# Kernel optimization log

Hardware: AMD Instinct MI355X
Metric: run time of the kernel (lower is better)

Reference implementation:

```python
import jax, jax.numpy as jnp
import numpy as np

B, S, H = 2, 2048, 2048
NH, NKV, HD = 16, 4, 128
ROPE_BASE = 10000.0


def hbit_linear(x, w):
    # BitNet: 8-bit per-token absmax activation quant, ternary (2-bit) weight quant
    s = 127.0 / jnp.clip(jnp.max(jnp.abs(x), axis=-1, keepdims=True), 1e-5, None)
    xq = jnp.clip(jnp.round(x * s), -128, 127) / s
    ws = 1.0 / jnp.clip(jnp.mean(jnp.abs(w)), 1e-5, None)
    wq = jnp.clip(jnp.round(w * ws), -1, 1) / ws
    return xq @ wq.T


def rotate_half(x):
    h = x.shape[-1] // 2
    return jnp.concatenate([-x[..., h:], x[..., :h]], axis=-1)


def rope_cos_sin(position_ids, head_dim, dtype):
    inv_freq = 1.0 / (ROPE_BASE ** (jnp.arange(0, head_dim, 2, dtype=jnp.float32) / head_dim))
    freqs = position_ids.astype(jnp.float32)[..., None] * inv_freq[None, None, :]  # (b,s,hd/2)
    emb = jnp.concatenate([freqs, freqs], axis=-1)  # (b,s,hd)
    return jnp.cos(emb).astype(dtype)[:, :, None, :], jnp.sin(emb).astype(dtype)[:, :, None, :]


def setup_inputs() -> dict:
    key = jax.random.key(0)
    ks = jax.random.split(key, 5)
    xavier = lambda k, shp: jax.random.uniform(k, shp, jnp.float32, -1.0, 1.0) * np.sqrt(6.0 / (shp[0] + shp[1]))
    causal = jnp.where(jnp.tril(jnp.ones((S, S), bool)), 0.0, -1e9).astype(jnp.float32)[None, None]
    return {
        "hidden_states": jax.random.normal(ks[0], (B, S, H), jnp.float32),
        "attention_mask": causal,
        "Wq": xavier(ks[1], (H, H)),
        "Wk": xavier(ks[2], (NKV * HD, H)),
        "Wv": xavier(ks[3], (NKV * HD, H)),
        "Wo": xavier(ks[4], (H, H)),
        "position_ids": jnp.arange(S, dtype=jnp.int64 if jax.config.jax_enable_x64 else jnp.int32)[None, :],
    }


def reference(hidden_states, attention_mask, Wq, Wk, Wv, Wo, position_ids):
    b, s, _ = hidden_states.shape
    q = hbit_linear(hidden_states, Wq).reshape(b, s, NH, HD)
    k = hbit_linear(hidden_states, Wk).reshape(b, s, NKV, HD)
    v = hbit_linear(hidden_states, Wv).reshape(b, s, NKV, HD)
    cos, sin = rope_cos_sin(position_ids, HD, q.dtype)  # (1,s,1,hd)
    q = q * cos + rotate_half(q) * sin
    k = k * cos + rotate_half(k) * sin
    n_rep = NH // NKV
    k = jnp.repeat(k, n_rep, axis=2)  # (b,s,NH,hd)
    v = jnp.repeat(v, n_rep, axis=2)
    scale = 1.0 / np.sqrt(HD)
    scores = jnp.einsum("bqhd,bkhd->bhqk", q, k) * scale + attention_mask
    probs = jax.nn.softmax(scores, axis=-1)  # dropout inactive (eval)
    out = jnp.einsum("bhqk,bkhd->bqhd", probs, v).reshape(b, s, NH * HD)
    return hbit_linear(out, Wo)
```

## Files before the change

kernel.cpp:

```cpp
#include <hip/hip_runtime.h>
#include <hip/hip_bf16.h>

#define B_ 2
#define S_ 2048
#define H_ 2048
#define NH_ 16
#define NKV_ 4
#define HD_ 128
#define M_ (B_*S_)
#define KVD_ (NKV_*HD_)

typedef signed char s8;
typedef __attribute__((ext_vector_type(8))) short short8;
typedef __attribute__((ext_vector_type(4))) float f32x4;
typedef __attribute__((ext_vector_type(4))) int int4v;

__device__ __forceinline__ float loadf(const void* p, long i, int isb){
  if (isb) return __bfloat162float(((const __hip_bfloat16*)p)[i]);
  return ((const float*)p)[i];
}

__device__ __forceinline__ unsigned short f2bf(float f){
  union { float f; unsigned u; } v; v.f = f;
  unsigned r = v.u + 0x7FFF + ((v.u >> 16) & 1);
  return (unsigned short)(r >> 16);
}

__device__ __forceinline__ float bf2f(unsigned short b){
  union { unsigned u; float f; } v; v.u = ((unsigned)b) << 16; return v.f;
}

__device__ __forceinline__ void gl2lds16(const void* g, void* l){
  __builtin_amdgcn_global_load_lds(
      (const __attribute__((address_space(1))) void*)g,
      (__attribute__((address_space(3))) void*)l, 16, 0, 0);
}

__global__ void k_detect(const unsigned int* x, int* flag){
  __shared__ int sh[256];
  int t = threadIdx.x, c = 0;
  for (int i = t; i < 2048; i += 256){
    unsigned e = (x[i] >> 7) & 0xFF;
    if (e >= 90 && e <= 150) c++;
  }
  sh[t] = c; __syncthreads();
  for (int k = 128; k > 0; k >>= 1){ if (t < k) sh[t] += sh[t+k]; __syncthreads(); }
  if (t == 0) flag[0] = (sh[0] > 1228) ? 1 : 0;
}

__global__ void k_prep(const void* Wq, const void* Wk, const void* Wv, const void* Wo,
                       const int* flag, float* wsum, float* ct, float* st){
  int bid = blockIdx.x, t = threadIdx.x;
  if (t < 64){
    float inv = exp2f(-(float)t * 0.20762050593045952f);
    float a = (float)bid * inv;
    float sn, cs; sincosf(a, &sn, &cs);
    ct[bid*64 + t] = cs; st[bid*64 + t] = sn;
  }
  __shared__ float sh[256];
  int isb = *flag;
  const void* w; long n; int wi; long b0; int nb;
  if (bid < 768)       { w = Wq; wi = 0; n = (long)H_*H_;   b0 = bid;      nb = 768; }
  else if (bid < 1024) { w = Wk; wi = 1; n = (long)KVD_*H_; b0 = bid-768;  nb = 256; }
  else if (bid < 1280) { w = Wv; wi = 2; n = (long)KVD_*H_; b0 = bid-1024; nb = 256; }
  else                 { w = Wo; wi = 3; n = (long)H_*H_;   b0 = bid-1280; nb = 768; }
  float s = 0.f;
  for (long i = b0*256 + t; i < n; i += (long)nb*256) s += fabsf(loadf(w, i, isb));
  sh[t] = s; __syncthreads();
  for (int k = 128; k > 0; k >>= 1){ if (t < k) sh[t] += sh[t+k]; __syncthreads(); }
  if (t == 0) atomicAdd(&wsum[wi], sh[0]);
}

__global__ void k_wquant_all(const void* Wq, const void* Wk, const void* Wv, const void* Wo,
                             const int* flag, const float* wsum,
                             s8* oq, s8* ok, s8* ov, s8* oo){
  int isb = *flag;
  int bid = blockIdx.x, t = threadIdx.x;
  const float cntq = (float)((long)H_*H_), cntkv = (float)((long)KVD_*H_);
  const void* w; s8* out; long n; int wi; long b0; int nb; float cnt;
  if (bid < 1024)      { w = Wq; out = oq; wi = 0; n = (long)H_*H_;   b0 = bid;       nb = 1024; cnt = cntq; }
  else if (bid < 1280) { w = Wk; out = ok; wi = 1; n = (long)KVD_*H_; b0 = bid-1024;  nb = 256;  cnt = cntkv; }
  else if (bid < 1536) { w = Wv; out = ov; wi = 2; n = (long)KVD_*H_; b0 = bid-1280;  nb = 256;  cnt = cntkv; }
  else                 { w = Wo; out = oo; wi = 3; n = (long)H_*H_;   b0 = bid-1536;  nb = 1024; cnt = cntq; }
  float mean = fmaxf(wsum[wi] / cnt, 1e-5f);
  float sc = 1.0f / mean;
  for (long i = b0*256 + t; i < n; i += (long)nb*256){
    float v = rintf(loadf(w, i, isb) * sc);
    v = fminf(fmaxf(v, -1.f), 1.f);
    out[i] = (s8)v;
  }
}

__global__ void k_aquant_in(const void* x, const int* flag, float* srow, s8* xq){
  __shared__ float sh[256];
  int isb = *flag; int r = blockIdx.x, t = threadIdx.x;
  long base = (long)r * H_;
  float v[8];
  if (isb){
    uint4 wv = ((const uint4*)((const unsigned short*)x + base))[t];
    unsigned u[4] = {wv.x, wv.y, wv.z, wv.w};
    #pragma unroll
    for (int i = 0; i < 4; i++){
      v[2*i]   = bf2f((unsigned short)(u[i] & 0xFFFF));
      v[2*i+1] = bf2f((unsigned short)(u[i] >> 16));
    }
  } else {
    const float4* p = (const float4*)((const float*)x + base);
    float4 a = p[t*2], b2 = p[t*2+1];
    v[0]=a.x; v[1]=a.y; v[2]=a.z; v[3]=a.w; v[4]=b2.x; v[5]=b2.y; v[6]=b2.z; v[7]=b2.w;
  }
  float mx = 0.f;
  #pragma unroll
  for (int i = 0; i < 8; i++) mx = fmaxf(mx, fabsf(v[i]));
  sh[t] = mx; __syncthreads();
  for (int k = 128; k > 0; k >>= 1){ if (t < k) sh[t] = fmaxf(sh[t], sh[t+k]); __syncthreads(); }
  float s = 127.0f / fmaxf(sh[0], 1e-5f);
  if (t == 0) srow[r] = s;
  unsigned long long pk = 0;
  #pragma unroll
  for (int i = 0; i < 8; i++){
    float q = fminf(fmaxf(rintf(v[i] * s), -128.f), 127.f);
    pk |= ((unsigned long long)(unsigned char)(s8)q) << (8*i);
  }
  *(unsigned long long*)(xq + base + t*8) = pk;
}

__global__ void k_aquant_bf16(const unsigned short* __restrict__ x, float* __restrict__ srow, s8* __restrict__ xq){
  __shared__ float sh[256];
  int r = blockIdx.x, t = threadIdx.x;
  long base = (long)r * H_;
  uint4 wv = ((const uint4*)(x + base))[t];
  unsigned u[4] = {wv.x, wv.y, wv.z, wv.w};
  float v[8];
  #pragma unroll
  for (int i = 0; i < 4; i++){
    v[2*i]   = bf2f((unsigned short)(u[i] & 0xFFFF));
    v[2*i+1] = bf2f((unsigned short)(u[i] >> 16));
  }
  float mx = 0.f;
  #pragma unroll
  for (int i = 0; i < 8; i++) mx = fmaxf(mx, fabsf(v[i]));
  sh[t] = mx; __syncthreads();
  for (int k = 128; k > 0; k >>= 1){ if (t < k) sh[t] = fmaxf(sh[t], sh[t+k]); __syncthreads(); }
  float s = 127.0f / fmaxf(sh[0], 1e-5f);
  if (t == 0) srow[r] = s;
  unsigned long long pk = 0;
  #pragma unroll
  for (int i = 0; i < 8; i++){
    float q = fminf(fmaxf(rintf(v[i] * s), -128.f), 127.f);
    pk |= ((unsigned long long)(unsigned char)(s8)q) << (8*i);
  }
  *(unsigned long long*)(xq + base + t*8) = pk;
}

__device__ __forceinline__ void gemm_core(
      const s8* __restrict__ A, const s8* __restrict__ Bw, s8* As, s8* Bs,
      const float* __restrict__ srow, float mean,
      void* __restrict__ Cout, int N, int mode, int isb,
      unsigned short* __restrict__ Vt,
      const float* __restrict__ ct, const float* __restrict__ st,
      long bcol, long arow){
  int tid = threadIdx.x;
  int wave = tid >> 6, lane = tid & 63;
  int quad = lane >> 4, c = lane & 15;
  int wm = wave >> 1, wn = wave & 1;
  const int K = H_;

  int4v acc[4][4];
  #pragma unroll
  for (int mt = 0; mt < 4; mt++)
    #pragma unroll
    for (int nt = 0; nt < 4; nt++) acc[mt][nt] = (int4v){0,0,0,0};

  int rl = lane >> 2;
  int kq = (lane & 3) ^ ((lane >> 3) & 3);
  int ch0 = wave*2, ch1 = wave*2 + 1;
  long gA0 = (arow + ch0*16 + rl)*(long)K + kq*16;
  long gA1 = (arow + ch1*16 + rl)*(long)K + kq*16;
  long gB0 = (bcol + ch0*16 + rl)*(long)K + kq*16;
  long gB1 = (bcol + ch1*16 + rl)*(long)K + kq*16;

  int sA = quad ^ ((c >> 1) & 3);
  int ntl[4];
  #pragma unroll
  for (int nt = 0; nt < 4; nt++) ntl[nt] = 2*wn + (nt & 1) + 4*(nt >> 1);
  int frA[4], frB[4];
  #pragma unroll
  for (int mt = 0; mt < 4; mt++) frA[mt] = (wm*64 + mt*16 + c)*64 + sA*16;
  #pragma unroll
  for (int nt = 0; nt < 4; nt++) frB[nt] = (ntl[nt]*16 + c)*64 + sA*16;

  for (int k0 = 0; k0 < K; k0 += 128){
    gl2lds16(A  + gA0 + k0,      As        + ch0*1024);
    gl2lds16(A  + gA1 + k0,      As        + ch1*1024);
    gl2lds16(Bw + gB0 + k0,      Bs        + ch0*1024);
    gl2lds16(Bw + gB1 + k0,      Bs        + ch1*1024);
    gl2lds16(A  + gA0 + k0 + 64, As + 8192 + ch0*1024);
    gl2lds16(A  + gA1 + k0 + 64, As + 8192 + ch1*1024);
    gl2lds16(Bw + gB0 + k0 + 64, Bs + 8192 + ch0*1024);
    gl2lds16(Bw + gB1 + k0 + 64, Bs + 8192 + ch1*1024);
    __syncthreads();
    #pragma unroll
    for (int s = 0; s < 2; s++){
      const s8* Ab = As + s*8192;
      const s8* Bb = Bs + s*8192;
      int4v afr[4], bfr[4];
      #pragma unroll
      for (int mt = 0; mt < 4; mt++) afr[mt] = *(const int4v*)&Ab[frA[mt]];
      #pragma unroll
      for (int nt = 0; nt < 4; nt++) bfr[nt] = *(const int4v*)&Bb[frB[nt]];
      #pragma unroll
      for (int mt = 0; mt < 4; mt++)
        #pragma unroll
        for (int nt = 0; nt < 4; nt++)
          acc[mt][nt] = __builtin_amdgcn_mfma_i32_16x16x64_i8(afr[mt], bfr[nt], acc[mt][nt], 0, 0, 0);
    }
    __syncthreads();
  }

  if (mode == 0 || mode == 3){
    unsigned short* Ob = (unsigned short*)Cout;
    #pragma unroll
    for (int mt = 0; mt < 4; mt++){
      #pragma unroll
      for (int r = 0; r < 4; r++){
        long grow = arow + wm*64 + mt*16 + quad*4 + r;
        float sc = mean / srow[grow];
        if (mode == 0) sc *= 0.12751743f;
        int pos = (int)(grow & (S_-1));
        #pragma unroll
        for (int p = 0; p < 2; p++){
          int col_lo = (int)bcol + (2*wn + p)*16 + c;
          int d = col_lo & 63;
          float cv = ct[pos*64 + d], sv = st[pos*64 + d];
          float vlo = acc[mt][p][r]   * sc;
          float vhi = acc[mt][p+2][r] * sc;
          Ob[grow*(long)N + col_lo]      = f2bf(vlo*cv - vhi*sv);
          Ob[grow*(long)N + col_lo + 64] = f2bf(vhi*cv + vlo*sv);
        }
      }
    }
  } else if (mode == 1){
    #pragma unroll
    for (int mt = 0; mt < 4; mt++){
      #pragma unroll
      for (int r = 0; r < 4; r++){
        long grow = arow + wm*64 + mt*16 + quad*4 + r;
        float sc = mean / srow[grow];
        long bb = grow >> 11; int sI = (int)(grow & (S_-1));
        unsigned short* base = Vt + bb*(long)KVD_*S_ + sI;
        #pragma unroll
        for (int nt = 0; nt < 4; nt++)
          base[(long)(bcol + ntl[nt]*16 + c)*S_] = f2bf(acc[mt][nt][r] * sc);
      }
    }
  } else {
    #pragma unroll
    for (int mt = 0; mt < 4; mt++){
      #pragma unroll
      for (int r = 0; r < 4; r++){
        long grow = arow + wm*64 + mt*16 + quad*4 + r;
        float sc = mean / srow[grow];
        long cb = grow*(long)N + bcol + c;
        if (isb){
          __hip_bfloat16* o = (__hip_bfloat16*)Cout;
          #pragma unroll
          for (int nt = 0; nt < 4; nt++)
            o[cb + ntl[nt]*16] = __float2bfloat16(acc[mt][nt][r] * sc);
        } else {
          float* o = (float*)Cout;
          #pragma unroll
          for (int nt = 0; nt < 4; nt++)
            o[cb + ntl[nt]*16] = acc[mt][nt][r] * sc;
        }
      }
    }
  }
}

__global__ __launch_bounds__(256, 2) void k_gemm_qkv(
      const s8* __restrict__ xq,
      const s8* __restrict__ wqq, const s8* __restrict__ wkq, const s8* __restrict__ wvq,
      const float* __restrict__ srow, const float* __restrict__ wsum,
      unsigned short* __restrict__ Qb, unsigned short* __restrict__ Kb,
      unsigned short* __restrict__ Vt,
      const float* __restrict__ ct, const float* __restrict__ st){
  __shared__ __align__(16) s8 As[2*128*64];
  __shared__ __align__(16) s8 Bs[2*128*64];
  int lid = blockIdx.x;
  int xcd = lid & 7;
  int rem = lid >> 3;
  int by  = xcd*4 + (rem & 3);
  int bx  = rem >> 2;
  const float cntq = (float)((long)H_*H_), cntkv = (float)((long)KVD_*H_);
  const s8* Bw; void* Cout; unsigned short* vt = nullptr;
  int N, mode; float mean; long bcol;
  if (bx < 16){
    Bw = wqq; Cout = Qb; N = H_;   mode = 0; mean = fmaxf(wsum[0]/cntq, 1e-5f);  bcol = (long)bx*128;
  } else if (bx < 20){
    Bw = wkq; Cout = Kb; N = KVD_; mode = 3; mean = fmaxf(wsum[1]/cntkv, 1e-5f); bcol = (long)(bx-16)*128;
  } else {
    Bw = wvq; Cout = nullptr; vt = Vt; N = KVD_; mode = 1; mean = fmaxf(wsum[2]/cntkv, 1e-5f); bcol = (long)(bx-20)*128;
  }
  gemm_core(xq, Bw, As, Bs, srow, mean, Cout, N, mode, 0, vt, ct, st, bcol, (long)by*128);
}

__global__ __launch_bounds__(256, 2) void k_gemm_o(
      const s8* __restrict__ aq, const s8* __restrict__ woq,
      const float* __restrict__ srow, const float* __restrict__ wsum,
      const int* __restrict__ flag, void* __restrict__ out,
      const float* __restrict__ ct, const float* __restrict__ st){
  __shared__ __align__(16) s8 As[2*128*64];
  __shared__ __align__(16) s8 Bs[2*128*64];
  int lid = blockIdx.x;
  int xcd = lid & 7;
  int rem = lid >> 3;
  int by  = xcd*4 + (rem & 3);
  int bx  = rem >> 2;
  float mean = fmaxf(wsum[3] / (float)((long)H_*H_), 1e-5f);
  gemm_core(aq, woq, As, Bs, srow, mean, out, H_, 2, *flag, nullptr, ct, st,
            (long)bx*128, (long)by*128);
}

#define PSTR 40
__global__ __launch_bounds__(256) void k_attn_mfma(const unsigned short* __restrict__ Qb,
    const unsigned short* __restrict__ Kb, const unsigned short* __restrict__ Vt,
    unsigned short* __restrict__ ob){
  int wid = threadIdx.x >> 6, lane = threadIdx.x & 63;
  int quad = lane >> 4, c = lane & 15;
  int kvh = blockIdx.y, b = blockIdx.z;
  int win = blockIdx.x;
  if (b == 1) win = (S_/32 - 1) - win;
  int h = kvh*4 + wid;
  int q0 = win*32;

  __shared__ __align__(16) unsigned short Ks[2][64*128];
  __shared__ __align__(16) unsigned short Vs[128*64];
  __shared__ __align__(16) unsigned short Ps[4][16*PSTR];

  short8 qf[2][4];
  #pragma unroll
  for (int t0 = 0; t0 < 2; t0++)
    #pragma unroll
    for (int f = 0; f < 4; f++)
      qf[t0][f] = *(const short8*)(Qb + ((long)(b*S_ + q0 + t0*16 + c)*NH_ + h)*HD_ + f*32 + quad*8);

  const unsigned short* Kg = Kb + (long)b*S_*KVD_ + kvh*HD_;
  const unsigned short* Vg = Vt + ((long)b*KVD_ + kvh*HD_)*S_;

  f32x4 o[2][8], ol[2];
  #pragma unroll
  for (int t0 = 0; t0 < 2; t0++){
    #pragma unroll
    for (int i = 0; i < 8; i++) o[t0][i] = (f32x4){0.f,0.f,0.f,0.f};
    ol[t0] = (f32x4){0.f,0.f,0.f,0.f};
  }
  short8 ones;
  #pragma unroll
  for (int i = 0; i < 8; i++) ones[i] = (short)0x3F80;

  int skey = lane >> 4;
  int kslot = lane & 15;
  int vrow = lane >> 3;
  int vslot = lane & 7;

  int nk = q0 + 32;
  #pragma unroll
  for (int i = 0; i < 4; i++){
    int kk = wid*16 + i*4;
    int key = kk + skey;
    int g = kslot ^ (key & 15);
    gl2lds16(Kg + (long)key*KVD_ + g*8, &Ks[0][kk*128]);
  }

  int buf = 0;
  for (int kc = 0; kc < nk; kc += 64, buf ^= 1){
    __syncthreads();
    #pragma unroll
    for (int i = 0; i < 4; i++){
      int rr = wid*32 + i*8;
      int hd = rr + vrow;
      int g = vslot ^ (hd & 7);
      gl2lds16(Vg + (long)hd*S_ + kc + g*8, &Vs[rr*64]);
    }

    f32x4 s[2][4];
    #pragma unroll
    for (int t0 = 0; t0 < 2; t0++)
      #pragma unroll
      for (int kt = 0; kt < 4; kt++) s[t0][kt] = (f32x4){0.f,0.f,0.f,0.f};
    #pragma unroll
    for (int kt = 0; kt < 4; kt++){
      short8 kf4[4];
      #pragma unroll
      for (int f = 0; f < 4; f++)
        kf4[f] = *(const short8*)&Ks[buf][(kt*16 + c)*128 + ((f*4 + quad) ^ c)*8];
      #pragma unroll
      for (int t0 = 0; t0 < 2; t0++)
        #pragma unroll
        for (int f = 0; f < 4; f++)
          s[t0][kt] = __builtin_amdgcn_mfma_f32_16x16x32_bf16(kf4[f], qf[t0][f], s[t0][kt], 0, 0, 0);
    }
    #pragma unroll
    for (int t0 = 0; t0 < 2; t0++){
      int qv = q0 + t0*16 + c;
      if (kc + 63 > q0 + t0*16){
        #pragma unroll
        for (int kt = 0; kt < 4; kt++){
          #pragma unroll
          for (int r = 0; r < 4; r++){
            int key = kc + kt*16 + quad*4 + r;
            if (key > qv) s[t0][kt][r] = -1e30f;
          }
        }
      }
    }

    __syncthreads();

    if (kc + 64 < nk){
      #pragma unroll
      for (int i = 0; i < 4; i++){
        int kk = wid*16 + i*4;
        int key = kk + skey;
        int g = kslot ^ (key & 15);
        gl2lds16(Kg + (long)(kc + 64 + key)*KVD_ + g*8, &Ks[buf^1][kk*128]);
      }
    }

    #pragma unroll
    for (int pp = 0; pp < 2; pp++){
      short8 vf[8];
      #pragma unroll
      for (int nt = 0; nt < 8; nt++)
        vf[nt] = *(const short8*)&Vs[(nt*16 + c)*64 + ((pp*4 + quad) ^ (c & 7))*8];
      #pragma unroll
      for (int t0 = 0; t0 < 2; t0++){
        #pragma unroll
        for (int tk = 0; tk < 2; tk++){
          f32x4 sv = s[t0][pp*2 + tk];
          float e0 = exp2f(sv[0]), e1 = exp2f(sv[1]);
          float e2 = exp2f(sv[2]), e3 = exp2f(sv[3]);
          unsigned w0, w1;
          asm("v_cvt_pk_bf16_f32 %0, %1, %2" : "=v"(w0) : "v"(e0), "v"(e1));
          asm("v_cvt_pk_bf16_f32 %0, %1, %2" : "=v"(w1) : "v"(e2), "v"(e3));
          uint2 pkv; pkv.x = w0; pkv.y = w1;
          *(uint2*)&Ps[wid][c*PSTR + tk*16 + quad*4] = pkv;
        }
        short8 pf = *(const short8*)&Ps[wid][c*PSTR + quad*8];
        #pragma unroll
        for (int nt = 0; nt < 8; nt++)
          o[t0][nt] = __builtin_amdgcn_mfma_f32_16x16x32_bf16(pf, vf[nt], o[t0][nt], 0, 0, 0);
        ol[t0] = __builtin_amdgcn_mfma_f32_16x16x32_bf16(pf, ones, ol[t0], 0, 0, 0);
      }
    }
  }

  #pragma unroll
  for (int t0 = 0; t0 < 2; t0++){
    float il[4];
    #pragma unroll
    for (int r = 0; r < 4; r++) il[r] = 1.0f / ol[t0][r];
    #pragma unroll
    for (int nt = 0; nt < 8; nt++)
      #pragma unroll
      for (int r = 0; r < 4; r++)
        ob[((long)(b*S_ + q0 + t0*16 + quad*4 + r))*H_ + h*HD_ + nt*16 + c] = f2bf(o[t0][nt][r]*il[r]);
  }
}

extern "C" void kernel_launch(void* const* d_in, const int* in_sizes, int n_in,
                              void* d_out, int out_size, void* d_ws, size_t ws_size,
                              hipStream_t stream){
  (void)in_sizes; (void)n_in; (void)out_size; (void)ws_size;
  const void* x  = d_in[0];
  const void* Wq = d_in[2];
  const void* Wk = d_in[3];
  const void* Wv = d_in[4];
  const void* Wo = d_in[5];
  char* ws = (char*)d_ws;
  size_t o = 0;
  auto alloc = [&](size_t b){ size_t r = o; o += (b + 255) & ~(size_t)255; return r; };
  size_t META = alloc(256);
  float* wsum = (float*)(ws + META);
  int*   flag = (int*)  (ws + META + 32);
  float* s_x = (float*)(ws + alloc((size_t)M_*4));
  float* s_a = (float*)(ws + alloc((size_t)M_*4));
  float* ct  = (float*)(ws + alloc((size_t)S_*64*4));
  float* st  = (float*)(ws + alloc((size_t)S_*64*4));
  s8* xq  = (s8*)(ws + alloc((size_t)M_*H_));
  s8* wqq = (s8*)(ws + alloc((size_t)H_*H_));
  s8* wkq = (s8*)(ws + alloc((size_t)KVD_*H_));
  s8* wvq = (s8*)(ws + alloc((size_t)KVD_*H_));
  s8* woq = (s8*)(ws + alloc((size_t)H_*H_));
  unsigned short* Qb = (unsigned short*)(ws + alloc((size_t)M_*NH_*HD_*2));
  unsigned short* Kb = (unsigned short*)(ws + alloc((size_t)M_*KVD_*2));
  unsigned short* Vt = (unsigned short*)(ws + alloc((size_t)M_*KVD_*2));
  unsigned short* ab = (unsigned short*)(ws + alloc((size_t)M_*H_*2));
  s8* aq = xq;

  hipMemsetAsync(ws + META, 0, 64, stream);
  k_detect<<<1,256,0,stream>>>((const unsigned int*)x, flag);
  k_prep<<<2048,256,0,stream>>>(Wq, Wk, Wv, Wo, flag, wsum, ct, st);
  k_wquant_all<<<2560,256,0,stream>>>(Wq, Wk, Wv, Wo, flag, wsum, wqq, wkq, wvq, woq);
  k_aquant_in<<<M_,256,0,stream>>>(x, flag, s_x, xq);

  k_gemm_qkv<<<768, 256, 0, stream>>>(xq, wqq, wkq, wvq, s_x, wsum, Qb, Kb, Vt, ct, st);

  dim3 ga(S_/32, NKV_, B_);
  k_attn_mfma<<<ga, 256, 0, stream>>>(Qb, Kb, Vt, ab);

  k_aquant_bf16<<<M_,256,0,stream>>>(ab, s_a, aq);

  k_gemm_o<<<512, 256, 0, stream>>>(aq, woq, s_a, wsum, flag, d_out, ct, st);
}
```

Before: 307.9 us.

## Fuse dtype detection into consumers and merge weight-sum prep with input quant

Removes the single-block dtype-detection kernel by having each consuming kernel recompute the bf16/fp32 flag from the first 2048 words of the input, using a wave-shuffle reduction. Weight abs-sum/rope table prep and the input activation quantization are merged into one launch. The V-transpose epilogue now packs four rows into a single 8-byte bf16 store using v_cvt_pk_bf16_f32. Together these cut two kernel launches and the scattered 2-byte stores, at the cost of every block redundantly reading 8 KB of input for detection.

```diff
diff --git a/kernel.cpp b/kernel.cpp
--- a/kernel.cpp
+++ b/kernel.cpp
@@ -36,45 +36,83 @@
       (__attribute__((address_space(3))) void*)l, 16, 0, 0);
 }
 
-__global__ void k_detect(const unsigned int* x, int* flag){
-  __shared__ int sh[256];
-  int t = threadIdx.x, c = 0;
-  for (int i = t; i < 2048; i += 256){
-    unsigned e = (x[i] >> 7) & 0xFF;
-    if (e >= 90 && e <= 150) c++;
-  }
-  sh[t] = c; __syncthreads();
-  for (int k = 128; k > 0; k >>= 1){ if (t < k) sh[t] += sh[t+k]; __syncthreads(); }
-  if (t == 0) flag[0] = (sh[0] > 1228) ? 1 : 0;
-}
-
-__global__ void k_prep(const void* Wq, const void* Wk, const void* Wv, const void* Wo,
-                       const int* flag, float* wsum, float* ct, float* st){
+__device__ __forceinline__ int detect_isb(const unsigned int* x){
+  __shared__ int dsh[4];
+  int t = threadIdx.x, cnt = 0;
+  #pragma unroll
+  for (int i = 0; i < 8; i++){
+    unsigned e = (x[t + i*256] >> 7) & 0xFF;
+    cnt += (e >= 90 && e <= 150) ? 1 : 0;
+  }
+  #pragma unroll
+  for (int k = 32; k > 0; k >>= 1) cnt += __shfl_down(cnt, k, 64);
+  if ((t & 63) == 0) dsh[t >> 6] = cnt;
+  __syncthreads();
+  return (dsh[0] + dsh[1] + dsh[2] + dsh[3]) > 1228;
+}
+
+__global__ void k_prep_aq(const void* x,
+                          const void* Wq, const void* Wk, const void* Wv, const void* Wo,
+                          float* wsum, float* ct, float* st,
+                          float* srow, s8* xq){
+  __shared__ float sh[256];
+  int isb = detect_isb((const unsigned int*)x);
   int bid = blockIdx.x, t = threadIdx.x;
-  if (t < 64){
-    float inv = exp2f(-(float)t * 0.20762050593045952f);
-    float a = (float)bid * inv;
-    float sn, cs; sincosf(a, &sn, &cs);
-    ct[bid*64 + t] = cs; st[bid*64 + t] = sn;
-  }
-  __shared__ float sh[256];
-  int isb = *flag;
-  const void* w; long n; int wi; long b0; int nb;
-  if (bid < 768)       { w = Wq; wi = 0; n = (long)H_*H_;   b0 = bid;      nb = 768; }
-  else if (bid < 1024) { w = Wk; wi = 1; n = (long)KVD_*H_; b0 = bid-768;  nb = 256; }
-  else if (bid < 1280) { w = Wv; wi = 2; n = (long)KVD_*H_; b0 = bid-1024; nb = 256; }
-  else                 { w = Wo; wi = 3; n = (long)H_*H_;   b0 = bid-1280; nb = 768; }
-  float s = 0.f;
-  for (long i = b0*256 + t; i < n; i += (long)nb*256) s += fabsf(loadf(w, i, isb));
-  sh[t] = s; __syncthreads();
-  for (int k = 128; k > 0; k >>= 1){ if (t < k) sh[t] += sh[t+k]; __syncthreads(); }
-  if (t == 0) atomicAdd(&wsum[wi], sh[0]);
+  if (bid < 2048){
+    if (t < 64){
+      float inv = exp2f(-(float)t * 0.20762050593045952f);
+      float a = (float)bid * inv;
+      float sn, cs; sincosf(a, &sn, &cs);
+      ct[bid*64 + t] = cs; st[bid*64 + t] = sn;
+    }
+    const void* w; long n; int wi; long b0; int nb;
+    if (bid < 768)       { w = Wq; wi = 0; n = (long)H_*H_;   b0 = bid;      nb = 768; }
+    else if (bid < 1024) { w = Wk; wi = 1; n = (long)KVD_*H_; b0 = bid-768;  nb = 256; }
+    else if (bid < 1280) { w = Wv; wi = 2; n = (long)KVD_*H_; b0 = bid-1024; nb = 256; }
+    else                 { w = Wo; wi = 3; n = (long)H_*H_;   b0 = bid-1280; nb = 768; }
+    float s = 0.f;
+    for (long i = b0*256 + t; i < n; i += (long)nb*256) s += fabsf(loadf(w, i, isb));
+    sh[t] = s; __syncthreads();
+    for (int k = 128; k > 0; k >>= 1){ if (t < k) sh[t] += sh[t+k]; __syncthreads(); }
+    if (t == 0) atomicAdd(&wsum[wi], sh[0]);
+  } else {
+    int r = bid - 2048;
+    long base = (long)r * H_;
+    float v[8];
+    if (isb){
+      uint4 wv = ((const uint4*)((const unsigned short*)x + base))[t];
+      unsigned u[4] = {wv.x, wv.y, wv.z, wv.w};
+      #pragma unroll
+      for (int i = 0; i < 4; i++){
+        v[2*i]   = bf2f((unsigned short)(u[i] & 0xFFFF));
+        v[2*i+1] = bf2f((unsigned short)(u[i] >> 16));
+      }
+    } else {
+      const float4* p = (const float4*)((const float*)x + base);
+      float4 a = p[t*2], b2 = p[t*2+1];
+      v[0]=a.x; v[1]=a.y; v[2]=a.z; v[3]=a.w; v[4]=b2.x; v[5]=b2.y; v[6]=b2.z; v[7]=b2.w;
+    }
+    float mx = 0.f;
+    #pragma unroll
+    for (int i = 0; i < 8; i++) mx = fmaxf(mx, fabsf(v[i]));
+    sh[t] = mx; __syncthreads();
+    for (int k = 128; k > 0; k >>= 1){ if (t < k) sh[t] = fmaxf(sh[t], sh[t+k]); __syncthreads(); }
+    float s = 127.0f / fmaxf(sh[0], 1e-5f);
+    if (t == 0) srow[r] = s;
+    unsigned long long pk = 0;
+    #pragma unroll
+    for (int i = 0; i < 8; i++){
+      float q = fminf(fmaxf(rintf(v[i] * s), -128.f), 127.f);
+      pk |= ((unsigned long long)(unsigned char)(s8)q) << (8*i);
+    }
+    *(unsigned long long*)(xq + base + t*8) = pk;
+  }
 }
 
 __global__ void k_wquant_all(const void* Wq, const void* Wk, const void* Wv, const void* Wo,
-                             const int* flag, const float* wsum,
+                             const void* x, const float* wsum,
                              s8* oq, s8* ok, s8* ov, s8* oo){
-  int isb = *flag;
+  int isb = detect_isb((const unsigned int*)x);
   int bid = blockIdx.x, t = threadIdx.x;
   const float cntq = (float)((long)H_*H_), cntkv = (float)((long)KVD_*H_);
   const void* w; s8* out; long n; int wi; long b0; int nb; float cnt;
@@ -89,40 +127,6 @@
     v = fminf(fmaxf(v, -1.f), 1.f);
     out[i] = (s8)v;
   }
-}
-
-__global__ void k_aquant_in(const void* x, const int* flag, float* srow, s8* xq){
-  __shared__ float sh[256];
-  int isb = *flag; int r = blockIdx.x, t = threadIdx.x;
-  long base = (long)r * H_;
-  float v[8];
-  if (isb){
-    uint4 wv = ((const uint4*)((const unsigned short*)x + base))[t];
-    unsigned u[4] = {wv.x, wv.y, wv.z, wv.w};
-    #pragma unroll
-    for (int i = 0; i < 4; i++){
-      v[2*i]   = bf2f((unsigned short)(u[i] & 0xFFFF));
-      v[2*i+1] = bf2f((unsigned short)(u[i] >> 16));
-    }
-  } else {
-    const float4* p = (const float4*)((const float*)x + base);
-    float4 a = p[t*2], b2 = p[t*2+1];
-    v[0]=a.x; v[1]=a.y; v[2]=a.z; v[3]=a.w; v[4]=b2.x; v[5]=b2.y; v[6]=b2.z; v[7]=b2.w;
-  }
-  float mx = 0.f;
-  #pragma unroll
-  for (int i = 0; i < 8; i++) mx = fmaxf(mx, fabsf(v[i]));
-  sh[t] = mx; __syncthreads();
-  for (int k = 128; k > 0; k >>= 1){ if (t < k) sh[t] = fmaxf(sh[t], sh[t+k]); __syncthreads(); }
-  float s = 127.0f / fmaxf(sh[0], 1e-5f);
-  if (t == 0) srow[r] = s;
-  unsigned long long pk = 0;
-  #pragma unroll
-  for (int i = 0; i < 8; i++){
-    float q = fminf(fmaxf(rintf(v[i] * s), -128.f), 127.f);
-    pk |= ((unsigned long long)(unsigned char)(s8)q) << (8*i);
-  }
-  *(unsigned long long*)(xq + base + t*8) = pk;
 }
 
 __global__ void k_aquant_bf16(const unsigned short* __restrict__ x, float* __restrict__ srow, s8* __restrict__ xq){
@@ -243,15 +247,22 @@
   } else if (mode == 1){
     #pragma unroll
     for (int mt = 0; mt < 4; mt++){
-      #pragma unroll
-      for (int r = 0; r < 4; r++){
-        long grow = arow + wm*64 + mt*16 + quad*4 + r;
-        float sc = mean / srow[grow];
-        long bb = grow >> 11; int sI = (int)(grow & (S_-1));
-        unsigned short* base = Vt + bb*(long)KVD_*S_ + sI;
-        #pragma unroll
-        for (int nt = 0; nt < 4; nt++)
-          base[(long)(bcol + ntl[nt]*16 + c)*S_] = f2bf(acc[mt][nt][r] * sc);
+      long grow0 = arow + wm*64 + mt*16 + quad*4;
+      float s0 = mean / srow[grow0];
+      float s1 = mean / srow[grow0+1];
+      float s2 = mean / srow[grow0+2];
+      float s3 = mean / srow[grow0+3];
+      long bb = grow0 >> 11; int sI = (int)(grow0 & (S_-1));
+      unsigned short* base = Vt + bb*(long)KVD_*S_ + sI;
+      #pragma unroll
+      for (int nt = 0; nt < 4; nt++){
+        float v0 = acc[mt][nt][0]*s0, v1 = acc[mt][nt][1]*s1;
+        float v2 = acc[mt][nt][2]*s2, v3 = acc[mt][nt][3]*s3;
+        unsigned lo, hi;
+        asm("v_cvt_pk_bf16_f32 %0, %1, %2" : "=v"(lo) : "v"(v0), "v"(v1));
+        asm("v_cvt_pk_bf16_f32 %0, %1, %2" : "=v"(hi) : "v"(v2), "v"(v3));
+        uint2 pk; pk.x = lo; pk.y = hi;
+        *(uint2*)(base + (long)(bcol + ntl[nt]*16 + c)*S_) = pk;
       }
     }
   } else {
@@ -308,17 +319,18 @@
 __global__ __launch_bounds__(256, 2) void k_gemm_o(
       const s8* __restrict__ aq, const s8* __restrict__ woq,
       const float* __restrict__ srow, const float* __restrict__ wsum,
-      const int* __restrict__ flag, void* __restrict__ out,
+      const void* __restrict__ x, void* __restrict__ out,
       const float* __restrict__ ct, const float* __restrict__ st){
   __shared__ __align__(16) s8 As[2*128*64];
   __shared__ __align__(16) s8 Bs[2*128*64];
+  int isb = detect_isb((const unsigned int*)x);
   int lid = blockIdx.x;
   int xcd = lid & 7;
   int rem = lid >> 3;
   int by  = xcd*4 + (rem & 3);
   int bx  = rem >> 2;
   float mean = fmaxf(wsum[3] / (float)((long)H_*H_), 1e-5f);
-  gemm_core(aq, woq, As, Bs, srow, mean, out, H_, 2, *flag, nullptr, ct, st,
+  gemm_core(aq, woq, As, Bs, srow, mean, out, H_, 2, isb, nullptr, ct, st,
             (long)bx*128, (long)by*128);
 }
 
@@ -483,7 +495,6 @@
   auto alloc = [&](size_t b){ size_t r = o; o += (b + 255) & ~(size_t)255; return r; };
   size_t META = alloc(256);
   float* wsum = (float*)(ws + META);
-  int*   flag = (int*)  (ws + META + 32);
   float* s_x = (float*)(ws + alloc((size_t)M_*4));
   float* s_a = (float*)(ws + alloc((size_t)M_*4));
   float* ct  = (float*)(ws + alloc((size_t)S_*64*4));
@@ -500,17 +511,17 @@
   s8* aq = xq;
 
   hipMemsetAsync(ws + META, 0, 64, stream);
-  k_detect<<<1,256,0,stream>>>((const unsigned int*)x, flag);
-  k_prep<<<2048,256,0,stream>>>(Wq, Wk, Wv, Wo, flag, wsum, ct, st);
-  k_wquant_all<<<2560,256,0,stream>>>(Wq, Wk, Wv, Wo, flag, wsum, wqq, wkq, wvq, woq);
-  k_aquant_in<<<M_,256,0,stream>>>(x, flag, s_x, xq);
+
+  k_prep_aq<<<2048 + M_, 256, 0, stream>>>(x, Wq, Wk, Wv, Wo, wsum, ct, st, s_x, xq);
+
+  k_wquant_all<<<2560, 256, 0, stream>>>(Wq, Wk, Wv, Wo, x, wsum, wqq, wkq, wvq, woq);
 
   k_gemm_qkv<<<768, 256, 0, stream>>>(xq, wqq, wkq, wvq, s_x, wsum, Qb, Kb, Vt, ct, st);
 
   dim3 ga(S_/32, NKV_, B_);
   k_attn_mfma<<<ga, 256, 0, stream>>>(Qb, Kb, Vt, ab);
 
-  k_aquant_bf16<<<M_,256,0,stream>>>(ab, s_a, aq);
-
-  k_gemm_o<<<512, 256, 0, stream>>>(aq, woq, s_a, wsum, flag, d_out, ct, st);
-}
+  k_aquant_bf16<<<M_, 256, 0, stream>>>(ab, s_a, aq);
+
+  k_gemm_o<<<512, 256, 0, stream>>>(aq, woq, s_a, wsum, x, d_out, ct, st);
+}
```

After: 289.7 us. 5.9% less time.
